# Performance work log

Hardware: AMD Instinct MI355X
Metric: run time of the kernel (lower is better)

## Reference

```python
import jax, jax.numpy as jnp
import numpy as np

# Dimensions
MAXN, MAXE = 4096, 8192
B, S, N, E = 8, 512, 1024, 2048
TYPE_DIM, MEM, TENC, EEMB, OUT = 16, 64, 32, 128, 64
MSG = TYPE_DIM + 2 * MEM + TENC + EEMB          # 304: GRU input dim
IN_GNN = EEMB + MEM                              # 192: TransformerConv in_channels
EDGE_DIM = TENC + EEMB                           # 160: TransformerConv edge_dim
# EVENT_TYPE_ID_MAP: pad=0, start=1, end=2, node-add=3, node-delete=4, edge-add=5, edge-delete=6


def setup_inputs() -> dict:
    key = jax.random.key(0)
    ks = jax.random.split(key, 32)
    ri = lambda i, shape, hi: jax.random.randint(ks[i], shape, 0, hi)
    rn = lambda i, shape, s=1.0: jax.random.normal(ks[i], shape, jnp.float32) * s
    ru = lambda i, shape: jax.random.uniform(ks[i], shape, dtype=jnp.float32)
    return {
        "event_type_ids": ri(0, (B, S), 7),
        "src_ids": ri(1, (B, S), MAXN),
        "src_mask": ru(2, (B, S)),
        "dst_ids": ri(3, (B, S), MAXN),
        "dst_mask": ru(4, (B, S)),
        "event_edge_ids": ri(5, (B, S), MAXE),
        "event_embeddings": rn(6, (B, S, EEMB)),
        "event_timestamps": ru(7, (B, S)),
        "node_ids": ri(8, (B, N), MAXN),
        "edge_ids": ri(9, (B, E), MAXE),
        "edge_index": ri(10, (B, 2, E), MAXN),
        "edge_timestamps": ru(11, (B, E)),
        "memory": rn(12, (MAXN, MEM), 0.1),
        "last_update": ru(13, (MAXE,)),
        "node_features": rn(14, (MAXN, EEMB), 0.1),
        "edge_features": rn(15, (MAXE, EEMB), 0.1),
        "type_emb": rn(16, (7, TYPE_DIM), 0.1),
        "time_w": rn(17, (TENC,), 0.1),
        "time_b": rn(18, (TENC,), 0.1),
        "gru_w_ih": rn(19, (3 * MEM, MSG), 0.05),
        "gru_w_hh": rn(20, (3 * MEM, MEM), 0.05),
        "gru_b_ih": rn(21, (3 * MEM,), 0.05),
        "gru_b_hh": rn(22, (3 * MEM,), 0.05),
        "Wq": rn(23, (OUT, IN_GNN), 0.05),
        "bq": rn(24, (OUT,), 0.05),
        "Wk": rn(25, (OUT, IN_GNN), 0.05),
        "bk": rn(26, (OUT,), 0.05),
        "Wv": rn(27, (OUT, IN_GNN), 0.05),
        "bv": rn(28, (OUT,), 0.05),
        "We": rn(29, (OUT, EDGE_DIM), 0.05),
        "Wskip": rn(30, (OUT, IN_GNN), 0.05),
        "bskip": rn(31, (OUT,), 0.05),
    }


def reference(event_type_ids, src_ids, src_mask, dst_ids, dst_mask, event_edge_ids,
              event_embeddings, event_timestamps, node_ids, edge_ids, edge_index,
              edge_timestamps, memory, last_update, node_features, edge_features,
              type_emb, time_w, time_b, gru_w_ih, gru_w_hh, gru_b_ih, gru_b_hh,
              Wq, bq, Wk, bk, Wv, bv, We, Wskip, bskip):
    f32 = jnp.float32
    time_enc = lambda t: jnp.cos(t[..., None] * time_w + time_b)  # TGN TimeEncoder: cos(Linear(t))

    # ---- message() ----
    type_embs = type_emb[event_type_ids]                      # (B,S,TYPE_DIM)
    src_embs = memory[src_ids] * src_mask[..., None]          # (B,S,MEM)
    dst_embs = memory[dst_ids] * dst_mask[..., None]
    rel_edge_ts = event_timestamps - last_update[event_edge_ids] * dst_mask
    is_node_ev = ((event_type_ids == 3) | (event_type_ids == 4)).astype(f32)
    not_special = (event_type_ids >= 3).astype(f32)           # not pad/start/end
    ts_emb = time_enc(event_timestamps * is_node_ev + rel_edge_ts * dst_mask) * not_special[..., None]
    src_msgs = jnp.concatenate([type_embs, src_embs, dst_embs, ts_emb, event_embeddings], -1) * not_special[..., None]
    dst_msgs = jnp.concatenate([type_embs, dst_embs, src_embs, ts_emb, event_embeddings], -1) * dst_mask[..., None]

    # ---- agg_message(): per-batch scatter-mean over node ids ----
    def seg_mean(m, ids):
        s = jax.ops.segment_sum(m, ids, num_segments=MAXN)
        c = jax.ops.segment_sum(jnp.ones(ids.shape, f32), ids, num_segments=MAXN)
        return s / jnp.maximum(c, 1.0)[:, None]
    # after flatten(end_dim=1), gathering by node id < MAXN picks from the batch-0 block
    agg_src0 = jax.vmap(seg_mean)(src_msgs, src_ids)[0]       # (MAXN, MSG)
    agg_dst0 = jax.vmap(seg_mean)(dst_msgs, dst_ids)[0]

    def gru(x, h):
        gi = x @ gru_w_ih.T + gru_b_ih
        gh = h @ gru_w_hh.T + gru_b_hh
        ir, iz, ic = jnp.split(gi, 3, -1)
        hr, hz, hc = jnp.split(gh, 3, -1)
        r = jax.nn.sigmoid(ir + hr)
        z = jax.nn.sigmoid(iz + hz)
        n = jnp.tanh(ic + r * hc)
        return (1.0 - z) * n + z * h

    present_src = jnp.zeros((MAXN,), bool).at[src_ids.ravel()].set(True)
    present_dst = jnp.zeros((MAXN,), bool).at[dst_ids.ravel()].set(True)
    mem_src = gru(agg_src0, memory)
    mem_dst = gru(agg_dst0, memory)
    mem = jnp.where(present_src[:, None], mem_src, memory)
    mem = jnp.where(present_dst[:, None], mem_dst, mem)

    # ---- GNN input prep ----
    rel_t_embs = time_enc(edge_timestamps - last_update[edge_ids])       # (B,E,TENC)
    x = jnp.concatenate([node_features[node_ids], mem[node_ids]], -1).reshape(B * N, IN_GNN)
    # localize_edge_index: first matching position of each edge id in flattened node_ids
    matches = node_ids.ravel()[:, None] == edge_index.ravel()[None, :]   # (B*N, B*2*E) bool
    loc = jnp.argmax(matches, axis=0).reshape(B, 2, E)                   # argmax = first True (0 if none)
    ei = loc.transpose(1, 0, 2).reshape(2, B * E)
    eattr = jnp.concatenate([rel_t_embs, edge_features[edge_ids]], -1).reshape(B * E, EDGE_DIM)

    # ---- TransformerConv (heads=1, root_weight=True, edge_dim set) ----
    q = x @ Wq.T + bq
    k = x @ Wk.T + bk
    v = x @ Wv.T + bv
    e = eattr @ We.T                                                     # lin_edge has no bias in PyG
    src, tgt = ei[0], ei[1]                                              # source_to_target flow
    k_e = k[src] + e
    v_e = v[src] + e
    score = jnp.sum(q[tgt] * k_e, -1) / np.float32(np.sqrt(OUT))
    m = jax.lax.stop_gradient(jax.ops.segment_max(score, tgt, num_segments=B * N))
    p = jnp.exp(score - m[tgt])
    den = jax.ops.segment_sum(p, tgt, num_segments=B * N)
    alpha = p / den[tgt]
    out = jax.ops.segment_sum(alpha[:, None] * v_e, tgt, num_segments=B * N)
    out = out + x @ Wskip.T + bskip
    return out.reshape(B, N, OUT)
```

## Files before the change

### kernel.cpp

```cpp
#include <hip/hip_runtime.h>
#include <math.h>

#define BB 8
#define SS 512
#define NEDGE 2048
#define MAXN 4096
#define TYPED 16
#define MEMD 64
#define TENC 32
#define EEMB 128
#define OUTD 64
#define MSG 304
#define INGNN 192
#define EDIM 160
#define BN 8192
#define BE 16384
#define QK_CH 96
#define EE_CH 80

__device__ __forceinline__ float sigmoidf(float x){ return 1.f/(1.f + expf(-x)); }

__global__ void k_init(float* zero_base, int n_zero, int* first_pos,
                       const float* Wq, const float* Wk, const float* Wv,
                       const float* Wskip, const float* We,
                       const float* bq, const float* bk,
                       const float* bv, const float* bskip,
                       float* WcatT, float* WeT, float* bcat){
  int i = blockIdx.x*blockDim.x + threadIdx.x;
  int stride = gridDim.x*blockDim.x;
  float4* z4 = (float4*)zero_base;
  int n4 = n_zero >> 2;
  float4 zero = {0.f,0.f,0.f,0.f};
  for (int t=i; t<n4; t+=stride) z4[t] = zero;
  for (int t=i; t<MAXN; t+=stride) first_pos[t] = 0x7FFFFFFF;
  int j = i;
  if (j < 4*64*192){
    int o = j/(64*192); int rem = j%(64*192); int q=rem/192, k=rem%192;
    const float* W = (o==0)?Wq:(o==1)?Wk:(o==2)?Wv:Wskip;
    WcatT[k*256 + o*64 + q] = W[rem];
  } else {
    j -= 4*64*192;
    if (j < 64*EDIM){ int q=j/EDIM, k=j%EDIM; WeT[k*64+q] = We[j]; }
    else {
      j -= 64*EDIM;
      if (j < 256){
        const float* b = (j<64)?bq:(j<128)?bk:(j<192)?bv:bskip;
        bcat[j] = b[j&63];
      }
    }
  }
}

__global__ void k_msg_first(const int* ev_type, const int* src_ids, const float* src_mask,
                            const int* dst_ids, const float* dst_mask, const int* ev_edge,
                            const float* ev_emb, const float* ev_ts, const float* memory,
                            const float* last_update, const float* type_emb,
                            const float* time_w, const float* time_b,
                            float* agg_src, float* agg_dst, int* cnt_src, int* cnt_dst,
                            const int* node_ids, int* first_pos, int* ps, int* pd){
  int bb = blockIdx.x;
  if (bb < SS){
    int s = bb;
    int et = ev_type[s];
    int sid = src_ids[s], did = dst_ids[s];
    float sm = src_mask[s], dm = dst_mask[s];
    float ts = ev_ts[s];
    float ns = (et >= 3) ? 1.f : 0.f;
    float ine = (et == 3 || et == 4) ? 1.f : 0.f;
    float rel = ts - last_update[ev_edge[s]] * dm;
    float tin = ts*ine + rel*dm;
    int d = threadIdx.x;
    if (d < MSG){
      float vs, vd;
      if (d < TYPED){ float t = type_emb[et*TYPED + d]; vs = t; vd = t; }
      else if (d < 80){ int c=d-16;  vs = memory[sid*MEMD+c]*sm; vd = memory[did*MEMD+c]*dm; }
      else if (d < 144){ int c=d-80; vs = memory[did*MEMD+c]*dm; vd = memory[sid*MEMD+c]*sm; }
      else if (d < 176){ int c=d-144; float ce = cosf(tin*time_w[c]+time_b[c])*ns; vs=ce; vd=ce; }
      else { float e = ev_emb[s*EEMB + (d-176)]; vs=e; vd=e; }
      atomicAdd(&agg_src[sid*MSG+d], vs*ns);
      atomicAdd(&agg_dst[did*MSG+d], vd*dm);
    }
    if (d == MSG){ atomicAdd(&cnt_src[sid], 1); atomicAdd(&cnt_dst[did], 1); }
  } else {
    int i = (bb - SS)*320 + threadIdx.x;
    if (i < BN) atomicMin(&first_pos[node_ids[i]], i);
    if (i < BB*SS){ ps[src_ids[i]] = 1; pd[dst_ids[i]] = 1; }
  }
}

__global__ __launch_bounds__(256) void k_gru_edge(
    const float* agg_src, const float* agg_dst, const int* cnt_src, const int* cnt_dst,
    const int* ps, const int* pd, const float* memory,
    const float* w_ih, const float* w_hh, const float* b_ih, const float* b_hh,
    float* mem_new,
    const int* edge_ids, const float* edge_ts, const float* last_update,
    const float* edge_features, const float* time_w, const float* time_b,
    const float* WeT, float* ebuf){
  __shared__ float smem[EE_CH*68 + EE_CH*64];
  int tid = threadIdx.x;
  if (blockIdx.x < 512){
    float* xs_t = smem;
    float* hs_t = smem + 3648;
    float* giL  = smem + 4416;
    float* ghL  = smem + 5952;
    int*   mode = (int*)(smem + 7488);
    float* rcnt = smem + 7496;
    int base = blockIdx.x * 8;
    if (tid < 8){
      int n = base + tid;
      int m = pd[n] ? 2 : (ps[n] ? 1 : 0);
      mode[tid] = m;
      int c = (m==2) ? cnt_dst[n] : ((m==1) ? cnt_src[n] : 0);
      rcnt[tid] = 1.f / (float)max(c, 1);
    }
    __syncthreads();
    for (int idx = tid; idx < 8*MSG; idx += 256){
      int t = idx / MSG, k = idx - t*MSG;
      const float* agg = (mode[t]==2) ? agg_dst : agg_src;
      xs_t[k*12 + t] = agg[(base+t)*MSG + k] * rcnt[t];
    }
    for (int idx = tid; idx < 8*MEMD; idx += 256){
      int t = idx / MEMD, k = idx - t*MEMD;
      hs_t[k*12 + t] = memory[(base+t)*MEMD + k];
    }
    __syncthreads();
    if (tid < 192){
      float4 a0={0,0,0,0}, a1={0,0,0,0};
      const float* wr = &w_ih[tid*MSG];
      #pragma unroll 2
      for (int k4 = 0; k4 < MSG; k4 += 4){
        float4 w4 = *(const float4*)&wr[k4];
        float4 x0, x1;
        x0 = *(const float4*)&xs_t[(k4+0)*12]; x1 = *(const float4*)&xs_t[(k4+0)*12+4];
        a0.x += w4.x*x0.x; a0.y += w4.x*x0.y; a0.z += w4.x*x0.z; a0.w += w4.x*x0.w;
        a1.x += w4.x*x1.x; a1.y += w4.x*x1.y; a1.z += w4.x*x1.z; a1.w += w4.x*x1.w;
        x0 = *(const float4*)&xs_t[(k4+1)*12]; x1 = *(const float4*)&xs_t[(k4+1)*12+4];
        a0.x += w4.y*x0.x; a0.y += w4.y*x0.y; a0.z += w4.y*x0.z; a0.w += w4.y*x0.w;
        a1.x += w4.y*x1.x; a1.y += w4.y*x1.y; a1.z += w4.y*x1.z; a1.w += w4.y*x1.w;
        x0 = *(const float4*)&xs_t[(k4+2)*12]; x1 = *(const float4*)&xs_t[(k4+2)*12+4];
        a0.x += w4.z*x0.x; a0.y += w4.z*x0.y; a0.z += w4.z*x0.z; a0.w += w4.z*x0.w;
        a1.x += w4.z*x1.x; a1.y += w4.z*x1.y; a1.z += w4.z*x1.z; a1.w += w4.z*x1.w;
        x0 = *(const float4*)&xs_t[(k4+3)*12]; x1 = *(const float4*)&xs_t[(k4+3)*12+4];
        a0.x += w4.w*x0.x; a0.y += w4.w*x0.y; a0.z += w4.w*x0.z; a0.w += w4.w*x0.w;
        a1.x += w4.w*x1.x; a1.y += w4.w*x1.y; a1.z += w4.w*x1.z; a1.w += w4.w*x1.w;
      }
      float bi = b_ih[tid];
      giL[0*192+tid]=a0.x+bi; giL[1*192+tid]=a0.y+bi; giL[2*192+tid]=a0.z+bi; giL[3*192+tid]=a0.w+bi;
      giL[4*192+tid]=a1.x+bi; giL[5*192+tid]=a1.y+bi; giL[6*192+tid]=a1.z+bi; giL[7*192+tid]=a1.w+bi;
      float4 b0={0,0,0,0}, b1={0,0,0,0};
      const float* wh = &w_hh[tid*MEMD];
      #pragma unroll 2
      for (int k4 = 0; k4 < MEMD; k4 += 4){
        float4 w4 = *(const float4*)&wh[k4];
        float4 x0, x1;
        x0 = *(const float4*)&hs_t[(k4+0)*12]; x1 = *(const float4*)&hs_t[(k4+0)*12+4];
        b0.x += w4.x*x0.x; b0.y += w4.x*x0.y; b0.z += w4.x*x0.z; b0.w += w4.x*x0.w;
        b1.x += w4.x*x1.x; b1.y += w4.x*x1.y; b1.z += w4.x*x1.z; b1.w += w4.x*x1.w;
        x0 = *(const float4*)&hs_t[(k4+1)*12]; x1 = *(const float4*)&hs_t[(k4+1)*12+4];
        b0.x += w4.y*x0.x; b0.y += w4.y*x0.y; b0.z += w4.y*x0.z; b0.w += w4.y*x0.w;
        b1.x += w4.y*x1.x; b1.y += w4.y*x1.y; b1.z += w4.y*x1.z; b1.w += w4.y*x1.w;
        x0 = *(const float4*)&hs_t[(k4+2)*12]; x1 = *(const float4*)&hs_t[(k4+2)*12+4];
        b0.x += w4.z*x0.x; b0.y += w4.z*x0.y; b0.z += w4.z*x0.z; b0.w += w4.z*x0.w;
        b1.x += w4.z*x1.x; b1.y += w4.z*x1.y; b1.z += w4.z*x1.z; b1.w += w4.z*x1.w;
        x0 = *(const float4*)&hs_t[(k4+3)*12]; x1 = *(const float4*)&hs_t[(k4+3)*12+4];
        b0.x += w4.w*x0.x; b0.y += w4.w*x0.y; b0.z += w4.w*x0.z; b0.w += w4.w*x0.w;
        b1.x += w4.w*x1.x; b1.y += w4.w*x1.y; b1.z += w4.w*x1.z; b1.w += w4.w*x1.w;
      }
      float bh = b_hh[tid];
      ghL[0*192+tid]=b0.x+bh; ghL[1*192+tid]=b0.y+bh; ghL[2*192+tid]=b0.z+bh; ghL[3*192+tid]=b0.w+bh;
      ghL[4*192+tid]=b1.x+bh; ghL[5*192+tid]=b1.y+bh; ghL[6*192+tid]=b1.z+bh; ghL[7*192+tid]=b1.w+bh;
    }
    __syncthreads();
    int cw = tid >> 6, col = tid & 63;
    for (int t = cw; t < 8; t += 4){
      float h = hs_t[col*12 + t];
      float outv;
      int m = mode[t];
      if (m == 0) outv = h;
      else {
        float r  = sigmoidf(giL[t*192+col]      + ghL[t*192+col]);
        float z  = sigmoidf(giL[t*192+64+col]   + ghL[t*192+64+col]);
        float ng = tanhf  (giL[t*192+128+col] + r*ghL[t*192+128+col]);
        outv = (1.f - z)*ng + z*h;
      }
      mem_new[(base+t)*MEMD + col] = outv;
    }
  } else {
    float* ea_t = smem;
    float* wls  = smem + EE_CH*68;
    int ebase = (blockIdx.x - 512) * 64;
    int ee = tid & 63, qq = tid >> 6;
    int j = ebase + ee;
    int eid = edge_ids[j];
    float rel = edge_ts[j] - last_update[eid];
    int tr = tid >> 4, tc = tid & 15;
    float4 acc[4];
    #pragma unroll
    for (int i=0;i<4;i++) acc[i] = (float4){0.f,0.f,0.f,0.f};
    for (int kc = 0; kc < 2; kc++){
      #pragma unroll 5
      for (int m = 0; m < 20; m++){
        int kk = qq*20 + m;
        int k  = kc*EE_CH + kk;
        float v = (k < TENC) ? cosf(rel*time_w[k] + time_b[k])
                             : edge_features[eid*EEMB + (k - TENC)];
        ea_t[kk*68 + ee] = v;
      }
      #pragma unroll
      for (int it = 0; it < 5; it++){
        int idx = tid + it*256;
        int kk = idx >> 4, c4 = (idx & 15) * 4;
        *(float4*)&wls[kk*64 + c4] = *(const float4*)&WeT[(kc*EE_CH + kk)*64 + c4];
      }
      __syncthreads();
      #pragma unroll 4
      for (int kk = 0; kk < EE_CH; kk++){
        float4 ev = *(const float4*)&ea_t[kk*68 + tr*4];
        float4 wv = *(const float4*)&wls[kk*64 + tc*4];
        acc[0].x += ev.x*wv.x; acc[0].y += ev.x*wv.y; acc[0].z += ev.x*wv.z; acc[0].w += ev.x*wv.w;
        acc[1].x += ev.y*wv.x; acc[1].y += ev.y*wv.y; acc[1].z += ev.y*wv.z; acc[1].w += ev.y*wv.w;
        acc[2].x += ev.z*wv.x; acc[2].y += ev.z*wv.y; acc[2].z += ev.z*wv.z; acc[2].w += ev.z*wv.w;
        acc[3].x += ev.w*wv.x; acc[3].y += ev.w*wv.y; acc[3].z += ev.w*wv.z; acc[3].w += ev.w*wv.w;
      }
      __syncthreads();
    }
    #pragma unroll
    for (int i=0;i<4;i++)
      *(float4*)&ebuf[(ebase + tr*4 + i)*OUTD + tc*4] = acc[i];
  }
}

__global__ __launch_bounds__(256) void k_qkvs(const int* node_ids, const float* node_feat,
                                              const float* mem_new, const float* WcatT,
                                              const float* bcat, float* qbuf, float* kbuf,
                                              float* vbuf, float* outbuf){
  __shared__ float smem[QK_CH*68 + QK_CH*64];
  float* xs_t = smem;
  float* wls  = smem + QK_CH*68;
  int tid = threadIdx.x;
  int rg = blockIdx.x >> 2, cgx = blockIdx.x & 3;
  int rbase = rg * 64;
  int rr = tid & 63, qq = tid >> 6;
  int nid = node_ids[rbase + rr];
  int tr = tid >> 4, tc = tid & 15;
  float4 acc[4];
  #pragma unroll
  for (int i=0;i<4;i++) acc[i] = (float4){0.f,0.f,0.f,0.f};
  for (int kc = 0; kc < 2; kc++){
    #pragma unroll 6
    for (int m = 0; m < 24; m++){
      int kk = qq*24 + m;
      int k  = kc*QK_CH + kk;
      float v = (k < EEMB) ? node_feat[nid*EEMB + k] : mem_new[nid*MEMD + (k-EEMB)];
      xs_t[kk*68 + rr] = v;
    }
    #pragma unroll
    for (int it = 0; it < 6; it++){
      int idx = tid + it*256;
      int kk = idx >> 4, c4 = (idx & 15) * 4;
      *(float4*)&wls[kk*64 + c4] = *(const float4*)&WcatT[(kc*QK_CH + kk)*256 + cgx*64 + c4];
    }
    __syncthreads();
    #pragma unroll 4
    for (int kk = 0; kk < QK_CH; kk++){
      float4 xv = *(const float4*)&xs_t[kk*68 + tr*4];
      float4 wv = *(const float4*)&wls[kk*64 + tc*4];
      acc[0].x += xv.x*wv.x; acc[0].y += xv.x*wv.y; acc[0].z += xv.x*wv.z; acc[0].w += xv.x*wv.w;
      acc[1].x += xv.y*wv.x; acc[1].y += xv.y*wv.y; acc[1].z += xv.y*wv.z; acc[1].w += xv.y*wv.w;
      acc[2].x += xv.z*wv.x; acc[2].y += xv.z*wv.y; acc[2].z += xv.z*wv.z; acc[2].w += xv.z*wv.w;
      acc[3].x += xv.w*wv.x; acc[3].y += xv.w*wv.y; acc[3].z += xv.w*wv.z; acc[3].w += xv.w*wv.w;
    }
    __syncthreads();
  }
  float4 b4 = *(const float4*)&bcat[cgx*64 + tc*4];
  float* dst = (cgx==0)? qbuf : (cgx==1)? kbuf : (cgx==2)? vbuf : outbuf;
  #pragma unroll
  for (int i=0;i<4;i++){
    float4 o = {acc[i].x+b4.x, acc[i].y+b4.y, acc[i].z+b4.z, acc[i].w+b4.w};
    *(float4*)&dst[(rbase + tr*4 + i)*OUTD + tc*4] = o;
  }
}

__global__ __launch_bounds__(256) void k_att(const int* edge_index, const int* first_pos,
                                             const float* qbuf, const float* kbuf,
                                             const float* vbuf, const float* ebuf,
                                             float* num, float* den,
                                             float* out0part, float* den0part){
  __shared__ float acc0[4][64];
  __shared__ float sdw[4];
  int tid = threadIdx.x;
  int w = tid >> 6, c = tid & 63;
  float a0 = 0.f, pden = 0.f;
  #pragma unroll
  for (int u = 0; u < 4; u++){
    int j = blockIdx.x*16 + w*4 + u;
    int b = j >> 11, e = j & (NEDGE-1);
    int vsrc = edge_index[b*2*NEDGE + e];
    int vtgt = edge_index[b*2*NEDGE + NEDGE + e];
    int fs = first_pos[vsrc]; if (fs == 0x7FFFFFFF) fs = 0;
    int ft = first_pos[vtgt]; if (ft == 0x7FFFFFFF) ft = 0;
    float ej = ebuf[j*OUTD + c];
    float partial = qbuf[ft*OUTD + c] * (kbuf[fs*OUTD + c] + ej);
    #pragma unroll
    for (int off = 32; off > 0; off >>= 1) partial += __shfl_down(partial, off, 64);
    float sc = __shfl(partial, 0, 64);
    float pe = expf(sc * 0.125f);
    float ve = vbuf[fs*OUTD + c] + ej;
    if (ft == 0){ a0 += pe*ve; pden += pe; }
    else {
      atomicAdd(&num[ft*OUTD + c], pe*ve);
      if (c == 0) atomicAdd(&den[ft], pe);
    }
  }
  acc0[w][c] = a0;
  if (c == 0) sdw[w] = pden;
  __syncthreads();
  if (w == 0){
    out0part[blockIdx.x*64 + c] = acc0[0][c]+acc0[1][c]+acc0[2][c]+acc0[3][c];
    if (c == 0) den0part[blockIdx.x] = sdw[0]+sdw[1]+sdw[2]+sdw[3];
  }
}

__global__ __launch_bounds__(256) void k_norm(const float* num, const float* den,
                                              const float* out0part, const float* den0part,
                                              float* out){
  int tid = threadIdx.x;
  if (blockIdx.x < 512){
    int r = blockIdx.x*16 + (tid >> 4);
    int c4 = (tid & 15) * 4;
    if (r > 0){
      float d = den[r];
      if (d > 0.f){
        float rinv = 1.f / d;
        float4 n4 = *(const float4*)&num[r*64 + c4];
        float4 o4 = *(const float4*)&out[r*64 + c4];
        o4.x += n4.x*rinv; o4.y += n4.y*rinv; o4.z += n4.z*rinv; o4.w += n4.w*rinv;
        *(float4*)&out[r*64 + c4] = o4;
      }
    }
  } else {
    __shared__ float part[4][64];
    __shared__ float dred[4];
    __shared__ float s_den0;
    int g = tid >> 6, c = tid & 63;
    float s = 0.f;
    for (int j = g*256; j < g*256 + 256; j++) s += out0part[j*64 + c];
    part[g][c] = s;
    float dd = den0part[tid] + den0part[tid+256] + den0part[tid+512] + den0part[tid+768];
    #pragma unroll
    for (int off = 32; off > 0; off >>= 1) dd += __shfl_down(dd, off, 64);
    if (c == 0) dred[g] = dd;
    __syncthreads();
    if (tid == 0) s_den0 = dred[0]+dred[1]+dred[2]+dred[3];
    __syncthreads();
    if (g == 0){
      float den0 = s_den0;
      if (den0 > 0.f)
        out[c] += (part[0][c]+part[1][c]+part[2][c]+part[3][c]) / den0;
    }
  }
}

extern "C" void kernel_launch(void* const* d_in, const int* in_sizes, int n_in,
                              void* d_out, int out_size, void* d_ws, size_t ws_size,
                              hipStream_t stream){
  const int*   ev_type      = (const int*)  d_in[0];
  const int*   src_ids      = (const int*)  d_in[1];
  const float* src_mask     = (const float*)d_in[2];
  const int*   dst_ids      = (const int*)  d_in[3];
  const float* dst_mask     = (const float*)d_in[4];
  const int*   ev_edge      = (const int*)  d_in[5];
  const float* ev_emb       = (const float*)d_in[6];
  const float* ev_ts        = (const float*)d_in[7];
  const int*   node_ids     = (const int*)  d_in[8];
  const int*   edge_ids     = (const int*)  d_in[9];
  const int*   edge_index   = (const int*)  d_in[10];
  const float* edge_ts      = (const float*)d_in[11];
  const float* memory       = (const float*)d_in[12];
  const float* last_update  = (const float*)d_in[13];
  const float* node_feat    = (const float*)d_in[14];
  const float* edge_feat    = (const float*)d_in[15];
  const float* type_emb     = (const float*)d_in[16];
  const float* time_w       = (const float*)d_in[17];
  const float* time_b       = (const float*)d_in[18];
  const float* gru_w_ih     = (const float*)d_in[19];
  const float* gru_w_hh     = (const float*)d_in[20];
  const float* gru_b_ih     = (const float*)d_in[21];
  const float* gru_b_hh     = (const float*)d_in[22];
  const float* Wq  = (const float*)d_in[23]; const float* bq    = (const float*)d_in[24];
  const float* Wk  = (const float*)d_in[25]; const float* bk    = (const float*)d_in[26];
  const float* Wv  = (const float*)d_in[27]; const float* bv    = (const float*)d_in[28];
  const float* We  = (const float*)d_in[29];
  const float* Wsk = (const float*)d_in[30]; const float* bskip = (const float*)d_in[31];
  float* out = (float*)d_out;

  float* ws = (float*)d_ws;
  size_t off = 0;
  float* agg_src = ws + off; off += (size_t)MAXN*MSG;
  float* agg_dst = ws + off; off += (size_t)MAXN*MSG;
  int* cnt_src   = (int*)(ws + off); off += MAXN;
  int* cnt_dst   = (int*)(ws + off); off += MAXN;
  int* present_s = (int*)(ws + off); off += MAXN;
  int* present_d = (int*)(ws + off); off += MAXN;
  float* den     = ws + off; off += BN;
  float* num     = ws + off; off += (size_t)BN*OUTD;
  int n_zero = (int)off;
  int* first_pos = (int*)(ws + off); off += MAXN;
  float* mem_new = ws + off; off += (size_t)MAXN*MEMD;
  float* qbuf    = ws + off; off += (size_t)BN*OUTD;
  float* kbuf    = ws + off; off += (size_t)BN*OUTD;
  float* vbuf    = ws + off; off += (size_t)BN*OUTD;
  float* ebuf    = ws + off; off += (size_t)BE*OUTD;
  float* den0part= ws + off; off += 1024;
  float* out0part= ws + off; off += 1024*64;
  float* WcatT   = ws + off; off += (size_t)INGNN*256;
  float* WeT     = ws + off; off += (size_t)EDIM*64;
  float* bcat    = ws + off; off += 256;

  k_init<<<2048, 256, 0, stream>>>(ws, n_zero, first_pos,
                                   Wq, Wk, Wv, Wsk, We, bq, bk, bv, bskip,
                                   WcatT, WeT, bcat);
  k_msg_first<<<SS + (BN + 319)/320, 320, 0, stream>>>(
      ev_type, src_ids, src_mask, dst_ids, dst_mask, ev_edge,
      ev_emb, ev_ts, memory, last_update, type_emb, time_w, time_b,
      agg_src, agg_dst, cnt_src, cnt_dst,
      node_ids, first_pos, present_s, present_d);
  k_gru_edge<<<768, 256, 0, stream>>>(agg_src, agg_dst, cnt_src, cnt_dst,
                                      present_s, present_d, memory,
                                      gru_w_ih, gru_w_hh, gru_b_ih, gru_b_hh, mem_new,
                                      edge_ids, edge_ts, last_update, edge_feat,
                                      time_w, time_b, WeT, ebuf);
  k_qkvs<<<512, 256, 0, stream>>>(node_ids, node_feat, mem_new, WcatT, bcat,
                                  qbuf, kbuf, vbuf, out);
  k_att<<<1024, 256, 0, stream>>>(edge_index, first_pos, qbuf, kbuf, vbuf, ebuf,
                                  num, den, out0part, den0part);
  k_norm<<<513, 256, 0, stream>>>(num, den, out0part, den0part, out);
}
```

Before: 79.18 us.

## Move edge projection into message kernel and give GRU its own 16-node-tile kernel

Moves the edge-attribute projection blocks out of the GRU kernel and into the message-scatter kernel, since they depend only on inputs. This lets that work run alongside the event atomics instead of alongside the GRU. The GRU becomes a standalone kernel that handles 16 nodes per block instead of 8, halving the number of weight-row passes per node. The cost is more shared memory and register pressure per GRU block and a smaller grid of 256 blocks.

```diff
diff --git a/kernel.cpp b/kernel.cpp
--- a/kernel.cpp
+++ b/kernel.cpp
@@ -17,6 +17,7 @@
 #define BE 16384
 #define QK_CH 96
 #define EE_CH 80
+#define GST 20
 
 __device__ __forceinline__ float sigmoidf(float x){ return 1.f/(1.f + expf(-x)); }
 
@@ -51,144 +52,23 @@
   }
 }
 
-__global__ void k_msg_first(const int* ev_type, const int* src_ids, const float* src_mask,
-                            const int* dst_ids, const float* dst_mask, const int* ev_edge,
-                            const float* ev_emb, const float* ev_ts, const float* memory,
-                            const float* last_update, const float* type_emb,
-                            const float* time_w, const float* time_b,
-                            float* agg_src, float* agg_dst, int* cnt_src, int* cnt_dst,
-                            const int* node_ids, int* first_pos, int* ps, int* pd){
-  int bb = blockIdx.x;
-  if (bb < SS){
-    int s = bb;
-    int et = ev_type[s];
-    int sid = src_ids[s], did = dst_ids[s];
-    float sm = src_mask[s], dm = dst_mask[s];
-    float ts = ev_ts[s];
-    float ns = (et >= 3) ? 1.f : 0.f;
-    float ine = (et == 3 || et == 4) ? 1.f : 0.f;
-    float rel = ts - last_update[ev_edge[s]] * dm;
-    float tin = ts*ine + rel*dm;
-    int d = threadIdx.x;
-    if (d < MSG){
-      float vs, vd;
-      if (d < TYPED){ float t = type_emb[et*TYPED + d]; vs = t; vd = t; }
-      else if (d < 80){ int c=d-16;  vs = memory[sid*MEMD+c]*sm; vd = memory[did*MEMD+c]*dm; }
-      else if (d < 144){ int c=d-80; vs = memory[did*MEMD+c]*dm; vd = memory[sid*MEMD+c]*sm; }
-      else if (d < 176){ int c=d-144; float ce = cosf(tin*time_w[c]+time_b[c])*ns; vs=ce; vd=ce; }
-      else { float e = ev_emb[s*EEMB + (d-176)]; vs=e; vd=e; }
-      atomicAdd(&agg_src[sid*MSG+d], vs*ns);
-      atomicAdd(&agg_dst[did*MSG+d], vd*dm);
-    }
-    if (d == MSG){ atomicAdd(&cnt_src[sid], 1); atomicAdd(&cnt_dst[did], 1); }
-  } else {
-    int i = (bb - SS)*320 + threadIdx.x;
-    if (i < BN) atomicMin(&first_pos[node_ids[i]], i);
-    if (i < BB*SS){ ps[src_ids[i]] = 1; pd[dst_ids[i]] = 1; }
-  }
-}
-
-__global__ __launch_bounds__(256) void k_gru_edge(
-    const float* agg_src, const float* agg_dst, const int* cnt_src, const int* cnt_dst,
-    const int* ps, const int* pd, const float* memory,
-    const float* w_ih, const float* w_hh, const float* b_ih, const float* b_hh,
-    float* mem_new,
-    const int* edge_ids, const float* edge_ts, const float* last_update,
-    const float* edge_features, const float* time_w, const float* time_b,
-    const float* WeT, float* ebuf){
+__global__ __launch_bounds__(256) void k_msg_edge(
+    const int* ev_type, const int* src_ids, const float* src_mask,
+    const int* dst_ids, const float* dst_mask, const int* ev_edge,
+    const float* ev_emb, const float* ev_ts, const float* memory,
+    const float* last_update, const float* type_emb,
+    const float* time_w, const float* time_b,
+    float* agg_src, float* agg_dst, int* cnt_src, int* cnt_dst,
+    const int* node_ids, int* first_pos, int* ps, int* pd,
+    const int* edge_ids, const float* edge_ts,
+    const float* edge_features, const float* WeT, float* ebuf){
   __shared__ float smem[EE_CH*68 + EE_CH*64];
   int tid = threadIdx.x;
-  if (blockIdx.x < 512){
-    float* xs_t = smem;
-    float* hs_t = smem + 3648;
-    float* giL  = smem + 4416;
-    float* ghL  = smem + 5952;
-    int*   mode = (int*)(smem + 7488);
-    float* rcnt = smem + 7496;
-    int base = blockIdx.x * 8;
-    if (tid < 8){
-      int n = base + tid;
-      int m = pd[n] ? 2 : (ps[n] ? 1 : 0);
-      mode[tid] = m;
-      int c = (m==2) ? cnt_dst[n] : ((m==1) ? cnt_src[n] : 0);
-      rcnt[tid] = 1.f / (float)max(c, 1);
-    }
-    __syncthreads();
-    for (int idx = tid; idx < 8*MSG; idx += 256){
-      int t = idx / MSG, k = idx - t*MSG;
-      const float* agg = (mode[t]==2) ? agg_dst : agg_src;
-      xs_t[k*12 + t] = agg[(base+t)*MSG + k] * rcnt[t];
-    }
-    for (int idx = tid; idx < 8*MEMD; idx += 256){
-      int t = idx / MEMD, k = idx - t*MEMD;
-      hs_t[k*12 + t] = memory[(base+t)*MEMD + k];
-    }
-    __syncthreads();
-    if (tid < 192){
-      float4 a0={0,0,0,0}, a1={0,0,0,0};
-      const float* wr = &w_ih[tid*MSG];
-      #pragma unroll 2
-      for (int k4 = 0; k4 < MSG; k4 += 4){
-        float4 w4 = *(const float4*)&wr[k4];
-        float4 x0, x1;
-        x0 = *(const float4*)&xs_t[(k4+0)*12]; x1 = *(const float4*)&xs_t[(k4+0)*12+4];
-        a0.x += w4.x*x0.x; a0.y += w4.x*x0.y; a0.z += w4.x*x0.z; a0.w += w4.x*x0.w;
-        a1.x += w4.x*x1.x; a1.y += w4.x*x1.y; a1.z += w4.x*x1.z; a1.w += w4.x*x1.w;
-        x0 = *(const float4*)&xs_t[(k4+1)*12]; x1 = *(const float4*)&xs_t[(k4+1)*12+4];
-        a0.x += w4.y*x0.x; a0.y += w4.y*x0.y; a0.z += w4.y*x0.z; a0.w += w4.y*x0.w;
-        a1.x += w4.y*x1.x; a1.y += w4.y*x1.y; a1.z += w4.y*x1.z; a1.w += w4.y*x1.w;
-        x0 = *(const float4*)&xs_t[(k4+2)*12]; x1 = *(const float4*)&xs_t[(k4+2)*12+4];
-        a0.x += w4.z*x0.x; a0.y += w4.z*x0.y; a0.z += w4.z*x0.z; a0.w += w4.z*x0.w;
-        a1.x += w4.z*x1.x; a1.y += w4.z*x1.y; a1.z += w4.z*x1.z; a1.w += w4.z*x1.w;
-        x0 = *(const float4*)&xs_t[(k4+3)*12]; x1 = *(const float4*)&xs_t[(k4+3)*12+4];
-        a0.x += w4.w*x0.x; a0.y += w4.w*x0.y; a0.z += w4.w*x0.z; a0.w += w4.w*x0.w;
-        a1.x += w4.w*x1.x; a1.y += w4.w*x1.y; a1.z += w4.w*x1.z; a1.w += w4.w*x1.w;
-      }
-      float bi = b_ih[tid];
-      giL[0*192+tid]=a0.x+bi; giL[1*192+tid]=a0.y+bi; giL[2*192+tid]=a0.z+bi; giL[3*192+tid]=a0.w+bi;
-      giL[4*192+tid]=a1.x+bi; giL[5*192+tid]=a1.y+bi; giL[6*192+tid]=a1.z+bi; giL[7*192+tid]=a1.w+bi;
-      float4 b0={0,0,0,0}, b1={0,0,0,0};
-      const float* wh = &w_hh[tid*MEMD];
-      #pragma unroll 2
-      for (int k4 = 0; k4 < MEMD; k4 += 4){
-        float4 w4 = *(const float4*)&wh[k4];
-        float4 x0, x1;
-        x0 = *(const float4*)&hs_t[(k4+0)*12]; x1 = *(const float4*)&hs_t[(k4+0)*12+4];
-        b0.x += w4.x*x0.x; b0.y += w4.x*x0.y; b0.z += w4.x*x0.z; b0.w += w4.x*x0.w;
-        b1.x += w4.x*x1.x; b1.y += w4.x*x1.y; b1.z += w4.x*x1.z; b1.w += w4.x*x1.w;
-        x0 = *(const float4*)&hs_t[(k4+1)*12]; x1 = *(const float4*)&hs_t[(k4+1)*12+4];
-        b0.x += w4.y*x0.x; b0.y += w4.y*x0.y; b0.z += w4.y*x0.z; b0.w += w4.y*x0.w;
-        b1.x += w4.y*x1.x; b1.y += w4.y*x1.y; b1.z += w4.y*x1.z; b1.w += w4.y*x1.w;
-        x0 = *(const float4*)&hs_t[(k4+2)*12]; x1 = *(const float4*)&hs_t[(k4+2)*12+4];
-        b0.x += w4.z*x0.x; b0.y += w4.z*x0.y; b0.z += w4.z*x0.z; b0.w += w4.z*x0.w;
-        b1.x += w4.z*x1.x; b1.y += w4.z*x1.y; b1.z += w4.z*x1.z; b1.w += w4.z*x1.w;
-        x0 = *(const float4*)&hs_t[(k4+3)*12]; x1 = *(const float4*)&hs_t[(k4+3)*12+4];
-        b0.x += w4.w*x0.x; b0.y += w4.w*x0.y; b0.z += w4.w*x0.z; b0.w += w4.w*x0.w;
-        b1.x += w4.w*x1.x; b1.y += w4.w*x1.y; b1.z += w4.w*x1.z; b1.w += w4.w*x1.w;
-      }
-      float bh = b_hh[tid];
-      ghL[0*192+tid]=b0.x+bh; ghL[1*192+tid]=b0.y+bh; ghL[2*192+tid]=b0.z+bh; ghL[3*192+tid]=b0.w+bh;
-      ghL[4*192+tid]=b1.x+bh; ghL[5*192+tid]=b1.y+bh; ghL[6*192+tid]=b1.z+bh; ghL[7*192+tid]=b1.w+bh;
-    }
-    __syncthreads();
-    int cw = tid >> 6, col = tid & 63;
-    for (int t = cw; t < 8; t += 4){
-      float h = hs_t[col*12 + t];
-      float outv;
-      int m = mode[t];
-      if (m == 0) outv = h;
-      else {
-        float r  = sigmoidf(giL[t*192+col]      + ghL[t*192+col]);
-        float z  = sigmoidf(giL[t*192+64+col]   + ghL[t*192+64+col]);
-        float ng = tanhf  (giL[t*192+128+col] + r*ghL[t*192+128+col]);
-        outv = (1.f - z)*ng + z*h;
-      }
-      mem_new[(base+t)*MEMD + col] = outv;
-    }
-  } else {
+  int bb = blockIdx.x;
+  if (bb < 256){
     float* ea_t = smem;
     float* wls  = smem + EE_CH*68;
-    int ebase = (blockIdx.x - 512) * 64;
+    int ebase = bb * 64;
     int ee = tid & 63, qq = tid >> 6;
     int j = ebase + ee;
     int eid = edge_ids[j];
@@ -227,6 +107,129 @@
     #pragma unroll
     for (int i=0;i<4;i++)
       *(float4*)&ebuf[(ebase + tr*4 + i)*OUTD + tc*4] = acc[i];
+  } else if (bb < 768){
+    int s = bb - 256;
+    int et = ev_type[s];
+    int sid = src_ids[s], did = dst_ids[s];
+    float sm = src_mask[s], dm = dst_mask[s];
+    float ts = ev_ts[s];
+    float ns = (et >= 3) ? 1.f : 0.f;
+    float ine = (et == 3 || et == 4) ? 1.f : 0.f;
+    float rel = ts - last_update[ev_edge[s]] * dm;
+    float tin = ts*ine + rel*dm;
+    for (int d = tid; d < MSG; d += 256){
+      float vs, vd;
+      if (d < TYPED){ float t = type_emb[et*TYPED + d]; vs = t; vd = t; }
+      else if (d < 80){ int c=d-16;  vs = memory[sid*MEMD+c]*sm; vd = memory[did*MEMD+c]*dm; }
+      else if (d < 144){ int c=d-80; vs = memory[did*MEMD+c]*dm; vd = memory[sid*MEMD+c]*sm; }
+      else if (d < 176){ int c=d-144; float ce = cosf(tin*time_w[c]+time_b[c])*ns; vs=ce; vd=ce; }
+      else { float e = ev_emb[s*EEMB + (d-176)]; vs=e; vd=e; }
+      atomicAdd(&agg_src[sid*MSG+d], vs*ns);
+      atomicAdd(&agg_dst[did*MSG+d], vd*dm);
+    }
+    if (tid == 0){ atomicAdd(&cnt_src[sid], 1); atomicAdd(&cnt_dst[did], 1); }
+  } else {
+    int i = (bb - 768)*256 + tid;
+    atomicMin(&first_pos[node_ids[i]], i);
+    if (i < BB*SS){ ps[src_ids[i]] = 1; pd[dst_ids[i]] = 1; }
+  }
+}
+
+__global__ __launch_bounds__(256) void k_gru(
+    const float* agg_src, const float* agg_dst, const int* cnt_src, const int* cnt_dst,
+    const int* ps, const int* pd, const float* memory,
+    const float* w_ih, const float* w_hh, const float* b_ih, const float* b_hh,
+    float* mem_new){
+  __shared__ float xs_t[MSG*GST];
+  __shared__ float hs_t[MEMD*GST];
+  __shared__ float giL[16*192];
+  __shared__ float ghL[16*192];
+  __shared__ int   mode[16];
+  __shared__ float rcnt[16];
+  int tid = threadIdx.x;
+  int base = blockIdx.x * 16;
+  if (tid < 16){
+    int n = base + tid;
+    int m = pd[n] ? 2 : (ps[n] ? 1 : 0);
+    mode[tid] = m;
+    int c = (m==2) ? cnt_dst[n] : ((m==1) ? cnt_src[n] : 0);
+    rcnt[tid] = 1.f / (float)max(c, 1);
+  }
+  __syncthreads();
+  for (int idx = tid; idx < 16*MSG; idx += 256){
+    int t = idx / MSG, k = idx - t*MSG;
+    const float* agg = (mode[t]==2) ? agg_dst : agg_src;
+    xs_t[k*GST + t] = agg[(base+t)*MSG + k] * rcnt[t];
+  }
+  for (int idx = tid; idx < 16*MEMD; idx += 256){
+    int t = idx >> 6, k = idx & 63;
+    hs_t[k*GST + t] = memory[(base+t)*MEMD + k];
+  }
+  __syncthreads();
+  if (tid < 192){
+    float4 A0={0,0,0,0}, A1={0,0,0,0}, A2={0,0,0,0}, A3={0,0,0,0};
+    const float* wr = &w_ih[tid*MSG];
+    #pragma unroll 2
+    for (int k4 = 0; k4 < MSG; k4 += 4){
+      float4 w4 = *(const float4*)&wr[k4];
+      #pragma unroll
+      for (int i = 0; i < 4; i++){
+        float wc = (i==0)? w4.x : (i==1)? w4.y : (i==2)? w4.z : w4.w;
+        const float* xb = &xs_t[(k4+i)*GST];
+        float4 x0 = *(const float4*)&xb[0];
+        float4 x1 = *(const float4*)&xb[4];
+        float4 x2 = *(const float4*)&xb[8];
+        float4 x3 = *(const float4*)&xb[12];
+        A0.x += wc*x0.x; A0.y += wc*x0.y; A0.z += wc*x0.z; A0.w += wc*x0.w;
+        A1.x += wc*x1.x; A1.y += wc*x1.y; A1.z += wc*x1.z; A1.w += wc*x1.w;
+        A2.x += wc*x2.x; A2.y += wc*x2.y; A2.z += wc*x2.z; A2.w += wc*x2.w;
+        A3.x += wc*x3.x; A3.y += wc*x3.y; A3.z += wc*x3.z; A3.w += wc*x3.w;
+      }
+    }
+    float bi = b_ih[tid];
+    giL[ 0*192+tid]=A0.x+bi; giL[ 1*192+tid]=A0.y+bi; giL[ 2*192+tid]=A0.z+bi; giL[ 3*192+tid]=A0.w+bi;
+    giL[ 4*192+tid]=A1.x+bi; giL[ 5*192+tid]=A1.y+bi; giL[ 6*192+tid]=A1.z+bi; giL[ 7*192+tid]=A1.w+bi;
+    giL[ 8*192+tid]=A2.x+bi; giL[ 9*192+tid]=A2.y+bi; giL[10*192+tid]=A2.z+bi; giL[11*192+tid]=A2.w+bi;
+    giL[12*192+tid]=A3.x+bi; giL[13*192+tid]=A3.y+bi; giL[14*192+tid]=A3.z+bi; giL[15*192+tid]=A3.w+bi;
+    float4 B0={0,0,0,0}, B1={0,0,0,0}, B2={0,0,0,0}, B3={0,0,0,0};
+    const float* wh = &w_hh[tid*MEMD];
+    #pragma unroll 2
+    for (int k4 = 0; k4 < MEMD; k4 += 4){
+      float4 w4 = *(const float4*)&wh[k4];
+      #pragma unroll
+      for (int i = 0; i < 4; i++){
+        float wc = (i==0)? w4.x : (i==1)? w4.y : (i==2)? w4.z : w4.w;
+        const float* xb = &hs_t[(k4+i)*GST];
+        float4 x0 = *(const float4*)&xb[0];
+        float4 x1 = *(const float4*)&xb[4];
+        float4 x2 = *(const float4*)&xb[8];
+        float4 x3 = *(const float4*)&xb[12];
+        B0.x += wc*x0.x; B0.y += wc*x0.y; B0.z += wc*x0.z; B0.w += wc*x0.w;
+        B1.x += wc*x1.x; B1.y += wc*x1.y; B1.z += wc*x1.z; B1.w += wc*x1.w;
+        B2.x += wc*x2.x; B2.y += wc*x2.y; B2.z += wc*x2.z; B2.w += wc*x2.w;
+        B3.x += wc*x3.x; B3.y += wc*x3.y; B3.z += wc*x3.z; B3.w += wc*x3.w;
+      }
+    }
+    float bh = b_hh[tid];
+    ghL[ 0*192+tid]=B0.x+bh; ghL[ 1*192+tid]=B0.y+bh; ghL[ 2*192+tid]=B0.z+bh; ghL[ 3*192+tid]=B0.w+bh;
+    ghL[ 4*192+tid]=B1.x+bh; ghL[ 5*192+tid]=B1.y+bh; ghL[ 6*192+tid]=B1.z+bh; ghL[ 7*192+tid]=B1.w+bh;
+    ghL[ 8*192+tid]=B2.x+bh; ghL[ 9*192+tid]=B2.y+bh; ghL[10*192+tid]=B2.z+bh; ghL[11*192+tid]=B2.w+bh;
+    ghL[12*192+tid]=B3.x+bh; ghL[13*192+tid]=B3.y+bh; ghL[14*192+tid]=B3.z+bh; ghL[15*192+tid]=B3.w+bh;
+  }
+  __syncthreads();
+  int cw = tid >> 6, col = tid & 63;
+  for (int t = cw; t < 16; t += 4){
+    float h = hs_t[col*GST + t];
+    float outv;
+    int m = mode[t];
+    if (m == 0) outv = h;
+    else {
+      float r  = sigmoidf(giL[t*192+col]      + ghL[t*192+col]);
+      float z  = sigmoidf(giL[t*192+64+col]   + ghL[t*192+64+col]);
+      float ng = tanhf  (giL[t*192+128+col] + r*ghL[t*192+128+col]);
+      outv = (1.f - z)*ng + z*h;
+    }
+    mem_new[(base+t)*MEMD + col] = outv;
   }
 }
 
@@ -420,16 +423,15 @@
   k_init<<<2048, 256, 0, stream>>>(ws, n_zero, first_pos,
                                    Wq, Wk, Wv, Wsk, We, bq, bk, bv, bskip,
                                    WcatT, WeT, bcat);
-  k_msg_first<<<SS + (BN + 319)/320, 320, 0, stream>>>(
+  k_msg_edge<<<800, 256, 0, stream>>>(
       ev_type, src_ids, src_mask, dst_ids, dst_mask, ev_edge,
       ev_emb, ev_ts, memory, last_update, type_emb, time_w, time_b,
       agg_src, agg_dst, cnt_src, cnt_dst,
-      node_ids, first_pos, present_s, present_d);
-  k_gru_edge<<<768, 256, 0, stream>>>(agg_src, agg_dst, cnt_src, cnt_dst,
-                                      present_s, present_d, memory,
-                                      gru_w_ih, gru_w_hh, gru_b_ih, gru_b_hh, mem_new,
-                                      edge_ids, edge_ts, last_update, edge_feat,
-                                      time_w, time_b, WeT, ebuf);
+      node_ids, first_pos, present_s, present_d,
+      edge_ids, edge_ts, edge_feat, WeT, ebuf);
+  k_gru<<<256, 256, 0, stream>>>(agg_src, agg_dst, cnt_src, cnt_dst,
+                                 present_s, present_d, memory,
+                                 gru_w_ih, gru_w_hh, gru_b_ih, gru_b_hh, mem_new);
   k_qkvs<<<512, 256, 0, stream>>>(node_ids, node_feat, mem_new, WcatT, bcat,
                                   qbuf, kbuf, vbuf, out);
   k_att<<<1024, 256, 0, stream>>>(edge_index, first_pos, qbuf, kbuf, vbuf, ebuf,
```

Measured after the change: 90.33 us. +14.1%, slower.
